# Kernel optimization log

Measured on AMD Instinct MI355X. Metric: run time of the kernel, lower is better.

Reference implementation:

```python
import jax, jax.numpy as jnp
import numpy as np
from jax import lax

DN = ('NCHW', 'OIHW', 'NCHW')

def _conv(x, w, b, stride):
    y = lax.conv_general_dilated(x, w, (stride, stride), [(1, 1), (1, 1)], dimension_numbers=DN)
    return y + b[None, :, None, None]

def _deconv(x, w, b):
    # ConvTranspose2d(k=4, stride=2, pad=1) == conv with lhs_dilation=2, pad=k-1-p=2,
    # with w already in flipped OIHW layout.
    y = lax.conv_general_dilated(x, w, (1, 1), [(2, 2), (2, 2)], lhs_dilation=(2, 2), dimension_numbers=DN)
    return y + b[None, :, None, None]

def setup_inputs() -> dict:
    key = jax.random.key(0)
    ks = jax.random.split(key, 14)
    s = 0.05  # keep activations numerically tame
    return {
        'x':   jax.random.normal(ks[0], (16, 3, 256, 256), jnp.float32),
        'ew1': jax.random.normal(ks[1], (64, 3, 4, 4), jnp.float32) * s,
        'eb1': jax.random.normal(ks[2], (64,), jnp.float32) * s,
        'ew2': jax.random.normal(ks[3], (128, 64, 4, 4), jnp.float32) * s,
        'eb2': jax.random.normal(ks[4], (128,), jnp.float32) * s,
        'ew3': jax.random.normal(ks[5], (256, 128, 4, 4), jnp.float32) * s,
        'eb3': jax.random.normal(ks[6], (256,), jnp.float32) * s,
        'cb':  jax.random.normal(ks[7], (8192, 256), jnp.float32),
        'dw1': jax.random.normal(ks[8], (128, 256, 4, 4), jnp.float32) * s,
        'db1': jax.random.normal(ks[9], (128,), jnp.float32) * s,
        'dw2': jax.random.normal(ks[10], (64, 128, 4, 4), jnp.float32) * s,
        'db2': jax.random.normal(ks[11], (64,), jnp.float32) * s,
        'dw3': jax.random.normal(ks[12], (3, 64, 4, 4), jnp.float32) * s,
        'db3': jax.random.normal(ks[13], (3,), jnp.float32) * s,
    }

def reference(x, ew1, eb1, ew2, eb2, ew3, eb3, cb, dw1, db1, dw2, db2, dw3, db3):
    # encoder: 3 stride-2 convs with ReLU between
    h = jax.nn.relu(_conv(x, ew1, eb1, 2))
    h = jax.nn.relu(_conv(h, ew2, eb2, 2))
    feat = _conv(h, ew3, eb3, 2)                     # [B, 256, 32, 32]
    B, C, H, W = feat.shape
    flat = feat.reshape(B, C, H * W).transpose(0, 2, 1)  # [B, HW, C]
    scores = jnp.einsum('btc,kc->btk', flat, cb)     # [B, HW, K] large matrix
    indices = jnp.argmax(scores, axis=-1)            # [B, HW]
    quantized = cb[indices]                          # [B, HW, C]
    q = quantized.transpose(0, 2, 1).reshape(B, C, H, W)
    # decoder: 3 stride-2 transposed convs with ReLU between
    d = jax.nn.relu(_deconv(q, dw1, db1))
    d = jax.nn.relu(_deconv(d, dw2, db2))
    recon = _deconv(d, dw3, db3)                     # [B, 3, 256, 256]
    return recon, indices
```

## Files before the change

kernel.cpp:

```cpp
#include <hip/hip_runtime.h>
#include <hip/hip_fp16.h>
#include <cstdint>
#include <cstddef>

typedef __attribute__((ext_vector_type(8))) short short8;
typedef __attribute__((ext_vector_type(8))) _Float16 h16x8;
typedef __attribute__((ext_vector_type(4))) float f32x4;

__device__ __forceinline__ short f2bf(float x) {
  union { float f; unsigned u; } a; a.f = x;
  unsigned r = a.u + 0x7fff + ((a.u >> 16) & 1);
  return (short)(r >> 16);
}
__device__ __forceinline__ float bf2f(short s) {
  union { unsigned u; float f; } a;
  a.u = ((unsigned)(unsigned short)s) << 16; return a.f;
}
__device__ __forceinline__ void fsplit16(float v, short& h, short& l) {
  __half a = __float2half(v);
  h = (short)__half_as_ushort(a);
  l = (short)__half_as_ushort(__float2half(v - __half2float(a)));
}

__device__ __forceinline__ void ld16(const void* g, void* l) {
  __builtin_amdgcn_global_load_lds(
      (const __attribute__((address_space(1))) unsigned int*)g,
      (__attribute__((address_space(3))) unsigned int*)l, 16, 0, 0);
}

__global__ __launch_bounds__(256) void conv1_kernel(
    const float* __restrict__ x, const float* __restrict__ w,
    const float* __restrict__ bias, short* __restrict__ yh, short* __restrict__ yl)
{
  __shared__ __align__(16) float wl[64 * 48];
  __shared__ float bl[64];
  const int tid = threadIdx.x;
  for (int i = tid; i < 64 * 48; i += 256) wl[i] = w[i];
  if (tid < 64) bl[tid] = bias[tid];
  __syncthreads();
  const int n  = blockIdx.y;
  const int oh = blockIdx.x * 2 + (tid >> 7);
  const int ow = tid & 127;
  const float* xb = x + (size_t)n * 3 * 65536;
  const int ih0 = oh * 2 - 1, iw0 = ow * 2 - 1;
  float xin[48];
#pragma unroll
  for (int ic = 0; ic < 3; ++ic)
#pragma unroll
    for (int kh = 0; kh < 4; ++kh) {
      int ih = ih0 + kh;
      bool rok = (unsigned)ih < 256u;
#pragma unroll
      for (int kw = 0; kw < 4; ++kw) {
        int iw = iw0 + kw;
        xin[ic * 16 + kh * 4 + kw] =
            (rok && (unsigned)iw < 256u) ? xb[ic * 65536 + ih * 256 + iw] : 0.f;
      }
    }
  const size_t ob = ((size_t)n * 16384 + oh * 128 + ow) * 64;
  for (int g = 0; g < 8; ++g) {
    short hs[8], ls[8];
#pragma unroll
    for (int j = 0; j < 8; ++j) {
      const int oc = g * 8 + j;
      float acc = bl[oc];
      const float* wo = &wl[oc * 48];
#pragma unroll
      for (int t = 0; t < 48; ++t) acc = fmaf(wo[t], xin[t], acc);
      acc = fmaxf(acc, 0.f) * 64.f;
      fsplit16(acc, hs[j], ls[j]);
    }
    *(short8*)(yh + ob + g * 8) = *(short8*)hs;
    *(short8*)(yl + ob + g * 8) = *(short8*)ls;
  }
}

template <int COUT, int CIN>
__global__ __launch_bounds__(256) void wpack_conv(
    const float* __restrict__ w, short* __restrict__ Wh, short* __restrict__ Wl)
{
  constexpr int K = 16 * CIN;
  const int idx = blockIdx.x * 256 + threadIdx.x;
  const int oc = idx / K, k = idx - oc * K;
  const int kk = k / CIN, ic = k - kk * CIN;
  const int kh = kk >> 2, kw = kk & 3;
  float v = w[(((size_t)oc * CIN + ic) * 4 + kh) * 4 + kw] * 64.f;
  short h, l;
  fsplit16(v, h, l);
  Wh[idx] = h;
  Wl[idx] = l;
}

template <int CIN, int HIN, int COUTT, bool RELU, bool OUTF>
__global__ __launch_bounds__(256) void conv_mfma(
    const short* __restrict__ inh, const short* __restrict__ inl,
    const short* __restrict__ Wph, const short* __restrict__ Wpl,
    const float* __restrict__ bias,
    short* __restrict__ outh, short* __restrict__ outl,
    float* __restrict__ outf)
{
  constexpr int K = 16 * CIN;
  constexpr int HOUT = HIN / 2;
  constexpr int MT = 128, NPX = 128;
  constexpr int GS = (HOUT == 64) ? 6 : 5;
  constexpr int AE = 4 * MT, BE = 4 * NPX;
  constexpr float RS = 1.f / 4096.f;
  __shared__ __align__(16) short AhL[AE * 8];
  __shared__ __align__(16) short AlL[AE * 8];
  __shared__ __align__(16) short BhL[BE * 8];
  __shared__ __align__(16) short BlL[BE * 8];
  __shared__ __align__(16) float bl[MT];
  const int tid = threadIdx.x;
  const int w = tid >> 6, lane = tid & 63;
  const int wm = w >> 1, wn = w & 1;
  const int kgl = lane >> 4, cl = lane & 15;
  const int n = blockIdx.z;
  const int oc0 = blockIdx.y * MT;
  const int oh0 = blockIdx.x * (NPX / HOUT);
  if (tid < MT) bl[tid] = bias[oc0 + tid];

  f32x4 acc[4][4];
#pragma unroll
  for (int i = 0; i < 4; ++i)
#pragma unroll
    for (int j = 0; j < 4; ++j) acc[i][j] = (f32x4){0.f, 0.f, 0.f, 0.f};

  for (int kc = 0; kc < K; kc += 32) {
    const int kk = kc / CIN, ic0 = kc % CIN;
    const int kh = kk >> 2, kw = kk & 3;
    __syncthreads();
#pragma unroll
    for (int rep = 0; rep < AE / 256; ++rep) {
      int e = rep * 256 + tid;
      int kg = e >> 7, oc_l = e & (MT - 1);
      size_t go = (size_t)(oc0 + oc_l) * K + kc + kg * 8;
      int lo = (e & ~63) * 8;
      ld16(Wph + go, AhL + lo);
      ld16(Wpl + go, AlL + lo);
    }
#pragma unroll
    for (int rep = 0; rep < BE / 256; ++rep) {
      int e = rep * 256 + tid;
      int kg = e >> 7, m = e & (NPX - 1);
      int ih = 2 * (oh0 + (m >> GS)) - 1 + kh;
      int iw = 2 * (m & (HOUT - 1)) - 1 + kw;
      bool ok = ((unsigned)ih < (unsigned)HIN) && ((unsigned)iw < (unsigned)HIN);
      size_t go = ok ? ((size_t)((n * HIN + ih) * HIN + iw) * CIN + ic0 + kg * 8)
                     : (size_t)(ic0 + kg * 8);
      int lo = (e & ~63) * 8;
      ld16(inh + go, BhL + lo);
      ld16(inl + go, BlL + lo);
    }
    __syncthreads();
    h16x8 ah[4], al[4], bh[4], blv[4];
#pragma unroll
    for (int mt = 0; mt < 4; ++mt) {
      int row = kgl * MT + wm * 64 + mt * 16 + cl;
      ah[mt] = *(const h16x8*)&AhL[row * 8];
      al[mt] = *(const h16x8*)&AlL[row * 8];
    }
    const h16x8 zz = {0, 0, 0, 0, 0, 0, 0, 0};
#pragma unroll
    for (int nt = 0; nt < 4; ++nt) {
      int m = wn * 64 + nt * 16 + cl;
      int row = kgl * NPX + m;
      h16x8 vh = *(const h16x8*)&BhL[row * 8];
      h16x8 vl = *(const h16x8*)&BlL[row * 8];
      int ih = 2 * (oh0 + (m >> GS)) - 1 + kh;
      int iw = 2 * (m & (HOUT - 1)) - 1 + kw;
      bool ok = ((unsigned)ih < (unsigned)HIN) && ((unsigned)iw < (unsigned)HIN);
      bh[nt] = ok ? vh : zz;
      blv[nt] = ok ? vl : zz;
    }
#pragma unroll
    for (int mt = 0; mt < 4; ++mt)
#pragma unroll
      for (int nt = 0; nt < 4; ++nt) {
        acc[mt][nt] = __builtin_amdgcn_mfma_f32_16x16x32_f16(
            ah[mt], bh[nt], acc[mt][nt], 0, 0, 0);
        acc[mt][nt] = __builtin_amdgcn_mfma_f32_16x16x32_f16(
            ah[mt], blv[nt], acc[mt][nt], 0, 0, 0);
        acc[mt][nt] = __builtin_amdgcn_mfma_f32_16x16x32_f16(
            al[mt], bh[nt], acc[mt][nt], 0, 0, 0);
      }
  }
#pragma unroll
  for (int mt = 0; mt < 4; ++mt) {
    const int oc = wm * 64 + mt * 16 + kgl * 4;
    const float4 bv = *(const float4*)&bl[oc];
#pragma unroll
    for (int nt = 0; nt < 4; ++nt) {
      const int px = wn * 64 + nt * 16 + cl;
      const int oh = oh0 + (px >> GS), ow = px & (HOUT - 1);
      const size_t ob =
          ((size_t)n * (HOUT * HOUT) + oh * HOUT + ow) * COUTT + oc0 + oc;
      float v0 = acc[mt][nt][0] * RS + bv.x;
      float v1 = acc[mt][nt][1] * RS + bv.y;
      float v2 = acc[mt][nt][2] * RS + bv.z;
      float v3 = acc[mt][nt][3] * RS + bv.w;
      if (RELU) {
        v0 = fmaxf(v0, 0.f); v1 = fmaxf(v1, 0.f);
        v2 = fmaxf(v2, 0.f); v3 = fmaxf(v3, 0.f);
      }
      if constexpr (OUTF) {
        ushort4 s;
        s.x = __half_as_ushort(__float2half(v0));
        s.y = __half_as_ushort(__float2half(v1));
        s.z = __half_as_ushort(__float2half(v2));
        s.w = __half_as_ushort(__float2half(v3));
        *(ushort4*)((unsigned short*)outh + ob) = s;
        *(float4*)(outf + ob) = make_float4(v0, v1, v2, v3);
      } else {
        short4 hh, ll;
        fsplit16(v0 * 64.f, hh.x, ll.x);
        fsplit16(v1 * 64.f, hh.y, ll.y);
        fsplit16(v2 * 64.f, hh.z, ll.z);
        fsplit16(v3 * 64.f, hh.w, ll.w);
        *(short4*)(outh + ob) = hh;
        *(short4*)(outl + ob) = ll;
      }
    }
  }
}

__global__ __launch_bounds__(256) void cb_convert(
    const float* __restrict__ cb, short* __restrict__ cbh,
    short* __restrict__ cbl, short* __restrict__ cb16)
{
  const int g = blockIdx.x * 256 + threadIdx.x;
  const float* p = cb + (size_t)g * 8;
  short hs[8], ls[8], fs[8];
#pragma unroll
  for (int u = 0; u < 8; ++u) {
    float v = p[u];
    short h = f2bf(v);
    hs[u] = h;
    ls[u] = f2bf(v - bf2f(h));
    fs[u] = (short)__half_as_ushort(__float2half(v));
  }
  *(short8*)(cbh + (size_t)g * 8) = *(short8*)hs;
  *(short8*)(cbl + (size_t)g * 8) = *(short8*)ls;
  *(short8*)(cb16 + (size_t)g * 8) = *(short8*)fs;
}

__global__ __launch_bounds__(256) void vq_mfma(
    const short* __restrict__ cb16, const short* __restrict__ ft16,
    float2* __restrict__ pval, int2* __restrict__ pidx)
{
  __shared__ __align__(16) short Ah[4 * 128 * 8];
  __shared__ __align__(16) short Bh[4 * 128 * 8];
  const int tid = threadIdx.x;
  const int w = tid >> 6, lane = tid & 63;
  const int wm = w >> 1, wn = w & 1;
  const int tg = blockIdx.x, cg = blockIdx.y;
  const int code0 = cg * 128, tok0 = tg * 128;
  const int kgl = lane >> 4, cl = lane & 15;

  f32x4 acc[4][4];
#pragma unroll
  for (int i = 0; i < 4; ++i)
#pragma unroll
    for (int j = 0; j < 4; ++j) acc[i][j] = (f32x4){0.f, 0.f, 0.f, 0.f};

  const int i0 = w * 128;
  for (int kc = 0; kc < 256; kc += 32) {
    __syncthreads();
#pragma unroll
    for (int rep = 0; rep < 2; ++rep) {
      int ib = i0 + rep * 64;
      int i = ib + lane;
      int m = i & 127, kg = i >> 7;
      size_t goffA = (size_t)(code0 + m) * 256 + kc + kg * 8;
      size_t goffB = (size_t)(tok0 + m) * 256 + kc + kg * 8;
      int loff = ib * 8;
      ld16(cb16 + goffA, Ah + loff);
      ld16(ft16 + goffB, Bh + loff);
    }
    __syncthreads();
    h16x8 ah[4], bh[4];
#pragma unroll
    for (int mt = 0; mt < 4; ++mt) {
      int row = wm * 64 + mt * 16 + cl;
      ah[mt] = *(const h16x8*)&Ah[(kgl * 128 + row) * 8];
    }
#pragma unroll
    for (int nt = 0; nt < 4; ++nt) {
      int row = wn * 64 + nt * 16 + cl;
      bh[nt] = *(const h16x8*)&Bh[(kgl * 128 + row) * 8];
    }
#pragma unroll
    for (int mt = 0; mt < 4; ++mt)
#pragma unroll
      for (int nt = 0; nt < 4; ++nt)
        acc[mt][nt] = __builtin_amdgcn_mfma_f32_16x16x32_f16(
            ah[mt], bh[nt], acc[mt][nt], 0, 0, 0);
  }
  __syncthreads();

  float* Sv = (float*)Ah;
  int* Si = (int*)Bh;
#pragma unroll
  for (int nt = 0; nt < 4; ++nt) {
    float v1 = -3.4e38f, v2 = -3.4e38f;
    int j1 = 0, j2 = 0;
#pragma unroll
    for (int mt = 0; mt < 4; ++mt) {
      int cb2 = code0 + wm * 64 + mt * 16 + kgl * 4;
      f32x4 a = acc[mt][nt];
#pragma unroll
      for (int r = 0; r < 4; ++r) {
        float val = a[r];
        int code = cb2 + r;
        if (val > v1) { v2 = v1; j2 = j1; v1 = val; j1 = code; }
        else if (val > v2) { v2 = val; j2 = code; }
      }
    }
    for (int mk = 16; mk < 64; mk <<= 1) {
      float ov1 = __shfl_xor(v1, mk);
      int oj1 = __shfl_xor(j1, mk);
      float ov2 = __shfl_xor(v2, mk);
      int oj2 = __shfl_xor(j2, mk);
      if (ov1 > v1) {
        if (v1 >= ov2) { v2 = v1; j2 = j1; } else { v2 = ov2; j2 = oj2; }
        v1 = ov1; j1 = oj1;
      } else if (ov1 > v2) { v2 = ov1; j2 = oj1; }
    }
    if (lane < 16) {
      int tl = wn * 64 + nt * 16 + lane;
      Sv[(wm * 128 + tl) * 2 + 0] = v1;
      Sv[(wm * 128 + tl) * 2 + 1] = v2;
      Si[(wm * 128 + tl) * 2 + 0] = j1;
      Si[(wm * 128 + tl) * 2 + 1] = j2;
    }
  }
  __syncthreads();
  if (tid < 128) {
    int tl = tid;
    float v1 = Sv[tl * 2], v2 = Sv[tl * 2 + 1];
    int j1 = Si[tl * 2], j2 = Si[tl * 2 + 1];
    float ov1 = Sv[(128 + tl) * 2], ov2 = Sv[(128 + tl) * 2 + 1];
    int oj1 = Si[(128 + tl) * 2], oj2 = Si[(128 + tl) * 2 + 1];
    if (ov1 > v1) {
      if (v1 >= ov2) { v2 = v1; j2 = j1; } else { v2 = ov2; j2 = oj2; }
      v1 = ov1; j1 = oj1;
    } else if (ov1 > v2) { v2 = ov1; j2 = oj1; }
    size_t o = (size_t)cg * 16384 + tok0 + tl;
    pval[o] = make_float2(v1, v2);
    pidx[o] = make_int2(j1, j2);
  }
}

__global__ __launch_bounds__(256) void vq_rescore(
    const float2* __restrict__ pval, const int2* __restrict__ pidx,
    const float* __restrict__ featc, const float* __restrict__ cb,
    int* __restrict__ fidx, float* __restrict__ idx_out)
{
  const int t = blockIdx.x * 256 + threadIdx.x;
  float vs[4] = {-3.4e38f, -3.4e38f, -3.4e38f, -3.4e38f};
  int is[4] = {0, 0, 0, 0};
  for (int cgi = 0; cgi < 64; ++cgi) {
    float2 pv = pval[(size_t)cgi * 16384 + t];
    int2 pi = pidx[(size_t)cgi * 16384 + t];
#pragma unroll
    for (int s = 0; s < 2; ++s) {
      float v = s ? pv.y : pv.x;
      int ii = s ? pi.y : pi.x;
      if (v > vs[3]) {
        vs[3] = v; is[3] = ii;
#pragma unroll
        for (int k = 3; k > 0; --k)
          if (vs[k] > vs[k - 1]) {
            float tv = vs[k]; vs[k] = vs[k - 1]; vs[k - 1] = tv;
            int ti = is[k]; is[k] = is[k - 1]; is[k - 1] = ti;
          }
      }
    }
  }
  const float4* fc = (const float4*)(featc + (size_t)t * 256);
  const float4* c0 = (const float4*)(cb + (size_t)is[0] * 256);
  const float4* c1 = (const float4*)(cb + (size_t)is[1] * 256);
  const float4* c2 = (const float4*)(cb + (size_t)is[2] * 256);
  const float4* c3 = (const float4*)(cb + (size_t)is[3] * 256);
  float s0 = 0.f, s1 = 0.f, s2 = 0.f, s3 = 0.f;
  for (int k4 = 0; k4 < 64; ++k4) {
    float4 f = fc[k4];
    float4 w0 = c0[k4], w1 = c1[k4], w2 = c2[k4], w3 = c3[k4];
    s0 = fmaf(w0.x, f.x, fmaf(w0.y, f.y, fmaf(w0.z, f.z, fmaf(w0.w, f.w, s0))));
    s1 = fmaf(w1.x, f.x, fmaf(w1.y, f.y, fmaf(w1.z, f.z, fmaf(w1.w, f.w, s1))));
    s2 = fmaf(w2.x, f.x, fmaf(w2.y, f.y, fmaf(w2.z, f.z, fmaf(w2.w, f.w, s2))));
    s3 = fmaf(w3.x, f.x, fmaf(w3.y, f.y, fmaf(w3.z, f.z, fmaf(w3.w, f.w, s3))));
  }
  float best = s0; int bi = is[0];
  float sv[3] = {s1, s2, s3};
  int si2[3] = {is[1], is[2], is[3]};
#pragma unroll
  for (int c = 0; c < 3; ++c)
    if (sv[c] > best || (sv[c] == best && si2[c] < bi)) { best = sv[c]; bi = si2[c]; }
  fidx[t] = bi;
  idx_out[t] = (float)bi;
}

template <int COUT, int CIN>
__global__ __launch_bounds__(256) void wpack(
    const float* __restrict__ w, short* __restrict__ Ah, short* __restrict__ Al)
{
  constexpr int K = 4 * CIN;
  const int idx = blockIdx.x * 256 + threadIdx.x;
  const int par = idx / (COUT * K);
  const int rem = idx % (COUT * K);
  const int oc = rem / K;
  const int k = rem % K;
  const int kk = k / CIN, ic = k % CIN;
  const int kh = 2 * (kk >> 1) + (par >> 1);
  const int kw = 2 * (kk & 1) + (par & 1);
  float v = w[(((size_t)oc * CIN + ic) * 4 + kh) * 4 + kw];
  short h = f2bf(v);
  Ah[idx] = h;
  Al[idx] = f2bf(v - bf2f(h));
}

__global__ __launch_bounds__(256) void zfill(float4* __restrict__ p) {
  p[threadIdx.x] = make_float4(0.f, 0.f, 0.f, 0.f);
}

__global__ __launch_bounds__(256) void gather2(
    const short* __restrict__ cbh, const short* __restrict__ cbl,
    const int* __restrict__ fidx, short* __restrict__ qTh, short* __restrict__ qTl)
{
  const int tid = threadIdx.x;
  const int gt = blockIdx.x * 64 + (tid >> 2);
  const int part = tid & 3;
  const int code = fidx[gt];
  const short8* sh = (const short8*)(cbh + (size_t)code * 256 + part * 64);
  const short8* sl = (const short8*)(cbl + (size_t)code * 256 + part * 64);
  short8* dh = (short8*)(qTh + (size_t)gt * 256 + part * 64);
  short8* dl = (short8*)(qTl + (size_t)gt * 256 + part * 64);
#pragma unroll
  for (int j = 0; j < 8; ++j) { dh[j] = sh[j]; dl[j] = sl[j]; }
}

template <int CIN, int GRID, int COUT, int NPX, int WM, int WN, bool OUT_HALF>
__global__ __launch_bounds__(256) void deconv_mfma(
    const short* __restrict__ inh, const short* __restrict__ inl,
    const short* __restrict__ Aph, const short* __restrict__ Apl,
    const float* __restrict__ bias, void* __restrict__ out_h,
    void* __restrict__ out_l, const short* __restrict__ zp)
{
  constexpr int K = 4 * CIN, HOUT = 2 * GRID, AE = 4 * COUT, BE = 4 * NPX;
  constexpr int GS = (GRID == 32) ? 5 : 6;
  __shared__ __align__(16) short AhL[AE * 8];
  __shared__ __align__(16) short AlL[AE * 8];
  __shared__ __align__(16) short BhL[BE * 8];
  __shared__ __align__(16) short BlL[BE * 8];
  __shared__ float bl[COUT];
  const int tid = threadIdx.x;
  const int w = tid >> 6, lane = tid & 63;
  const int wm = w / WN, wn = w % WN;
  const int kgl = lane >> 4, cl = lane & 15;
  const int par = blockIdx.y, n = blockIdx.z;
  const int pr = par >> 1, pc = par & 1;
  const int Ut0 = blockIdx.x * (NPX / GRID);
  if (tid < COUT) bl[tid] = bias[tid];

  f32x4 acc[4][4];
#pragma unroll
  for (int i = 0; i < 4; ++i)
#pragma unroll
    for (int j = 0; j < 4; ++j) acc[i][j] = (f32x4){0.f, 0.f, 0.f, 0.f};

  for (int kc = 0; kc < K; kc += 32) {
    const int kk = kc / CIN, ic0 = kc % CIN;
    const int dr = (kk >> 1) + pr - 1, dc = (kk & 1) + pc - 1;
    __syncthreads();
#pragma unroll
    for (int rep = 0; rep < AE / 256; ++rep) {
      int e = rep * 256 + tid;
      int kg = e / COUT, oc_l = e % COUT;
      size_t go = ((size_t)(par * COUT + oc_l)) * K + kc + kg * 8;
      int lo = (e & ~63) * 8;
      ld16(Aph + go, AhL + lo);
      ld16(Apl + go, AlL + lo);
    }
#pragma unroll
    for (int rep = 0; rep < BE / 256; ++rep) {
      int e = rep * 256 + tid;
      int kg = e / NPX, m = e % NPX;
      int sU = Ut0 + (m >> GS) + dr;
      int sV = (m & (GRID - 1)) + dc;
      bool ok = (unsigned)sU < (unsigned)GRID && (unsigned)sV < (unsigned)GRID;
      long pix = (long)(n * GRID + sU) * GRID + sV;
      size_t go = (size_t)(pix * CIN + ic0 + kg * 8);
      int lo = (e & ~63) * 8;
      ld16(ok ? inh + go : zp, BhL + lo);
      ld16(ok ? inl + go : zp, BlL + lo);
    }
    __syncthreads();
    short8 ah[4], al[4], bh[4], blo[4];
#pragma unroll
    for (int mt = 0; mt < 4; ++mt) {
      int row = kgl * COUT + wm * 64 + mt * 16 + cl;
      ah[mt] = *(const short8*)&AhL[row * 8];
      al[mt] = *(const short8*)&AlL[row * 8];
    }
#pragma unroll
    for (int nt = 0; nt < 4; ++nt) {
      int row = kgl * NPX + wn * 64 + nt * 16 + cl;
      bh[nt] = *(const short8*)&BhL[row * 8];
      blo[nt] = *(const short8*)&BlL[row * 8];
    }
#pragma unroll
    for (int mt = 0; mt < 4; ++mt)
#pragma unroll
      for (int nt = 0; nt < 4; ++nt) {
        acc[mt][nt] = __builtin_amdgcn_mfma_f32_16x16x32_bf16(
            ah[mt], bh[nt], acc[mt][nt], 0, 0, 0);
        acc[mt][nt] = __builtin_amdgcn_mfma_f32_16x16x32_bf16(
            ah[mt], blo[nt], acc[mt][nt], 0, 0, 0);
        acc[mt][nt] = __builtin_amdgcn_mfma_f32_16x16x32_bf16(
            al[mt], bh[nt], acc[mt][nt], 0, 0, 0);
      }
  }
#pragma unroll
  for (int mt = 0; mt < 4; ++mt) {
    const int oc = wm * 64 + mt * 16 + kgl * 4;
    const float4 bv = *(const float4*)&bl[oc];
#pragma unroll
    for (int nt = 0; nt < 4; ++nt) {
      const int px = wn * 64 + nt * 16 + cl;
      const int U = Ut0 + (px >> GS), V = px & (GRID - 1);
      const int r = 2 * U + pr, c = 2 * V + pc;
      const size_t ob = ((size_t)n * HOUT * HOUT + (size_t)r * HOUT + c) * COUT + oc;
      float v0 = fmaxf(acc[mt][nt][0] + bv.x, 0.f);
      float v1 = fmaxf(acc[mt][nt][1] + bv.y, 0.f);
      float v2 = fmaxf(acc[mt][nt][2] + bv.z, 0.f);
      float v3 = fmaxf(acc[mt][nt][3] + bv.w, 0.f);
      if constexpr (OUT_HALF) {
        ushort4 s;
        s.x = __half_as_ushort(__float2half(v0));
        s.y = __half_as_ushort(__float2half(v1));
        s.z = __half_as_ushort(__float2half(v2));
        s.w = __half_as_ushort(__float2half(v3));
        *(ushort4*)((unsigned short*)out_h + ob) = s;
      } else {
        short4 hh, ll;
        hh.x = f2bf(v0); ll.x = f2bf(v0 - bf2f(hh.x));
        hh.y = f2bf(v1); ll.y = f2bf(v1 - bf2f(hh.y));
        hh.z = f2bf(v2); ll.z = f2bf(v2 - bf2f(hh.z));
        hh.w = f2bf(v3); ll.w = f2bf(v3 - bf2f(hh.w));
        *(short4*)((short*)out_h + ob) = hh;
        *(short4*)((short*)out_l + ob) = ll;
      }
    }
  }
}

__global__ __launch_bounds__(256) void deconv3_kernel(
    const __half* __restrict__ d2, const float* __restrict__ w,
    const float* __restrict__ bias, float* __restrict__ y)
{
  __shared__ __align__(16) float Xl[108 * 68];
  __shared__ __align__(16) float wl[4 * 4 * 3 * 64];
  const int tid = threadIdx.x;
  for (int i = tid; i < 3072; i += 256) {
    int oc = i >> 10, ic = (i >> 4) & 63, kh = (i >> 2) & 3, kw = i & 3;
    int par = (kh & 1) * 2 + (kw & 1), kidx = (kh >> 1) * 2 + (kw >> 1);
    wl[((par * 4 + kidx) * 3 + oc) * 64 + ic] = w[i];
  }
  const int n = blockIdx.z, r0 = blockIdx.y * 8, c0 = blockIdx.x * 32;
  const int gr0 = (r0 >> 1) - 1, gc0 = (c0 >> 1) - 1;
  for (int e = tid; e < 1728; e += 256) {
    int pl = e >> 4, sub = e & 15;
    int rr = pl / 18, cc = pl - rr * 18;
    int gr = gr0 + rr, gc = gc0 + cc;
    float4 v = make_float4(0.f, 0.f, 0.f, 0.f);
    if ((unsigned)gr < 128u && (unsigned)gc < 128u) {
      const __half2* p =
          (const __half2*)(d2 + ((size_t)(n * 16384 + gr * 128 + gc) * 64 + sub * 4));
      float2 f0 = __half22float2(p[0]);
      float2 f1 = __half22float2(p[1]);
      v = make_float4(f0.x, f0.y, f1.x, f1.y);
    }
    *(float4*)&Xl[pl * 68 + sub * 4] = v;
  }
  __syncthreads();
  const int wv = tid >> 6, lane = tid & 63;
  const int pr = wv >> 1, pc = wv & 1;
  const int Ul = lane >> 4, Vl = lane & 15;
  float a0 = bias[0], a1 = bias[1], a2 = bias[2];
  const int parb = wv * 768;
#pragma unroll
  for (int ic4 = 0; ic4 < 16; ++ic4) {
    float4 xv[4];
#pragma unroll
    for (int t = 0; t < 4; ++t) {
      int lr = Ul + (t >> 1) + pr, lc = Vl + (t & 1) + pc;
      xv[t] = *(const float4*)&Xl[(lr * 18 + lc) * 68 + ic4 * 4];
    }
#pragma unroll
    for (int t = 0; t < 4; ++t) {
      float4 w0 = *(const float4*)&wl[parb + (t * 3 + 0) * 64 + ic4 * 4];
      float4 w1 = *(const float4*)&wl[parb + (t * 3 + 1) * 64 + ic4 * 4];
      float4 w2 = *(const float4*)&wl[parb + (t * 3 + 2) * 64 + ic4 * 4];
      a0 = fmaf(w0.x, xv[t].x, fmaf(w0.y, xv[t].y, fmaf(w0.z, xv[t].z, fmaf(w0.w, xv[t].w, a0))));
      a1 = fmaf(w1.x, xv[t].x, fmaf(w1.y, xv[t].y, fmaf(w1.z, xv[t].z, fmaf(w1.w, xv[t].w, a1))));
      a2 = fmaf(w2.x, xv[t].x, fmaf(w2.y, xv[t].y, fmaf(w2.z, xv[t].z, fmaf(w2.w, xv[t].w, a2))));
    }
  }
  const int r = r0 + 2 * Ul + pr, c = c0 + 2 * Vl + pc;
  float* yn = y + (size_t)n * 3 * 65536 + r * 256 + c;
  yn[0] = a0;
  yn[65536] = a1;
  yn[131072] = a2;
}

extern "C" void kernel_launch(void* const* d_in, const int* in_sizes, int n_in,
                              void* d_out, int out_size, void* d_ws, size_t ws_size,
                              hipStream_t stream)
{
  const float* x   = (const float*)d_in[0];
  const float* ew1 = (const float*)d_in[1];
  const float* eb1 = (const float*)d_in[2];
  const float* ew2 = (const float*)d_in[3];
  const float* eb2 = (const float*)d_in[4];
  const float* ew3 = (const float*)d_in[5];
  const float* eb3 = (const float*)d_in[6];
  const float* cb  = (const float*)d_in[7];
  const float* dw1 = (const float*)d_in[8];
  const float* db1 = (const float*)d_in[9];
  const float* dw2 = (const float*)d_in[10];
  const float* db2 = (const float*)d_in[11];
  const float* dw3 = (const float*)d_in[12];
  const float* db3 = (const float*)d_in[13];

  float* recon = (float*)d_out;
  float* idxf  = (float*)d_out + 3145728;

  const size_t MB = 1048576ull;
  char* ws = (char*)d_ws;
  short* h1h = (short*)ws;
  short* h1l = (short*)(ws + 32 * MB);
  short* h2h = (short*)(ws + 64 * MB);
  short* h2l = (short*)(ws + 80 * MB);
  short* ft16  = (short*)ws;
  float* featf = (float*)(ws + 16 * MB);
  short* cbh  = (short*)(ws + 64 * MB);
  short* cbl  = (short*)(ws + 68 * MB);
  short* cb16 = (short*)(ws + 72 * MB);
  float2* pval = (float2*)(ws + 76 * MB);
  int2*   pidx = (int2*)(ws + 84 * MB);
  int*    fidx = (int*)(ws + 92 * MB);
  short* A1h = (short*)(ws + 76 * MB);
  short* A1l = (short*)(ws + 77 * MB);
  short* A2h = (short*)(ws + 78 * MB);
  short* A2l = (short*)(ws + 78 * MB + 262144);
  short* zp  = (short*)(ws + 78 * MB + 524288);
  short* qTh = (short*)ws;
  short* qTl = (short*)(ws + 8 * MB);
  short* d1h = (short*)(ws + 32 * MB);
  short* d1l = (short*)(ws + 48 * MB);
  __half* d2 = (__half*)ws;
  short* W2h = (short*)recon;
  short* W2l = W2h + 131072;
  short* W3h = W2h + 262144;
  short* W3l = W2h + 786432;

  conv1_kernel<<<dim3(64, 16), 256, 0, stream>>>(x, ew1, eb1, h1h, h1l);
  wpack_conv<128, 64><<<dim3(512), 256, 0, stream>>>(ew2, W2h, W2l);
  conv_mfma<64, 128, 128, true, false><<<dim3(32, 1, 16), 256, 0, stream>>>(
      h1h, h1l, W2h, W2l, eb2, h2h, h2l, nullptr);
  wpack_conv<256, 128><<<dim3(2048), 256, 0, stream>>>(ew3, W3h, W3l);
  conv_mfma<128, 64, 256, false, true><<<dim3(8, 2, 16), 256, 0, stream>>>(
      h2h, h2l, W3h, W3l, eb3, ft16, nullptr, featf);

  cb_convert<<<dim3(1024), 256, 0, stream>>>(cb, cbh, cbl, cb16);
  vq_mfma<<<dim3(128, 64), 256, 0, stream>>>(cb16, ft16, pval, pidx);
  vq_rescore<<<dim3(64), 256, 0, stream>>>(pval, pidx, featf, cb, fidx, idxf);

  wpack<128, 256><<<dim3(2048), 256, 0, stream>>>(dw1, A1h, A1l);
  wpack<64, 128><<<dim3(512), 256, 0, stream>>>(dw2, A2h, A2l);
  zfill<<<dim3(1), 256, 0, stream>>>((float4*)zp);
  gather2<<<dim3(256), 256, 0, stream>>>(cbh, cbl, fidx, qTh, qTl);

  deconv_mfma<256, 32, 128, 128, 2, 2, false>
      <<<dim3(8, 4, 16), 256, 0, stream>>>(qTh, qTl, A1h, A1l, db1, d1h, d1l, zp);
  deconv_mfma<128, 64, 64, 256, 1, 4, true>
      <<<dim3(16, 4, 16), 256, 0, stream>>>(d1h, d1l, A2h, A2l, db2, d2, d2, zp);
  deconv3_kernel<<<dim3(8, 32, 16), 256, 0, stream>>>(d2, dw3, db3, recon);
}
```

Measured before the change: 900.9 us.

## Double-buffer weight tiles and load activations directly into registers in MFMA convs

The conv, deconv and VQ MFMA kernels now keep two shared-memory buffers for the weight/codebook tiles, so the next K-slice is loaded while the current one is computed, with one barrier per stage instead of two. In the conv and deconv kernels the activation (B) operand no longer goes through shared memory; each lane reads its fragments straight from global memory into registers and zeroes out-of-bounds taps. This also removes the zero-page buffer and its zfill launch. The cost is more registers and more shared memory per block, and uncoalesced, repeated global reads of activations that may lower occupancy or raise memory traffic.

```diff
diff --git a/kernel.cpp b/kernel.cpp
--- a/kernel.cpp
+++ b/kernel.cpp
@@ -103,12 +103,11 @@
   constexpr int HOUT = HIN / 2;
   constexpr int MT = 128, NPX = 128;
   constexpr int GS = (HOUT == 64) ? 6 : 5;
-  constexpr int AE = 4 * MT, BE = 4 * NPX;
+  constexpr int AE = 4 * MT;
+  constexpr int NS = K / 32;
   constexpr float RS = 1.f / 4096.f;
-  __shared__ __align__(16) short AhL[AE * 8];
-  __shared__ __align__(16) short AlL[AE * 8];
-  __shared__ __align__(16) short BhL[BE * 8];
-  __shared__ __align__(16) short BlL[BE * 8];
+  __shared__ __align__(16) short AhL[2][AE * 8];
+  __shared__ __align__(16) short AlL[2][AE * 8];
   __shared__ __align__(16) float bl[MT];
   const int tid = threadIdx.x;
   const int w = tid >> 6, lane = tid & 63;
@@ -125,52 +124,44 @@
 #pragma unroll
     for (int j = 0; j < 4; ++j) acc[i][j] = (f32x4){0.f, 0.f, 0.f, 0.f};
 
-  for (int kc = 0; kc < K; kc += 32) {
-    const int kk = kc / CIN, ic0 = kc % CIN;
-    const int kh = kk >> 2, kw = kk & 3;
-    __syncthreads();
+  auto stageA = [&](int s, int b) {
+    const int kc = s * 32;
 #pragma unroll
     for (int rep = 0; rep < AE / 256; ++rep) {
       int e = rep * 256 + tid;
       int kg = e >> 7, oc_l = e & (MT - 1);
       size_t go = (size_t)(oc0 + oc_l) * K + kc + kg * 8;
       int lo = (e & ~63) * 8;
-      ld16(Wph + go, AhL + lo);
-      ld16(Wpl + go, AlL + lo);
-    }
-#pragma unroll
-    for (int rep = 0; rep < BE / 256; ++rep) {
-      int e = rep * 256 + tid;
-      int kg = e >> 7, m = e & (NPX - 1);
+      ld16(Wph + go, &AhL[b][lo]);
+      ld16(Wpl + go, &AlL[b][lo]);
+    }
+  };
+  const h16x8 zzh = {0, 0, 0, 0, 0, 0, 0, 0};
+  auto loadB = [&](int s, h16x8* bh, h16x8* blv) {
+    const int kc = s * 32;
+    const int kk = kc / CIN, ic0 = kc % CIN;
+    const int kh = kk >> 2, kw = kk & 3;
+#pragma unroll
+    for (int nt = 0; nt < 4; ++nt) {
+      int m = wn * 64 + nt * 16 + cl;
       int ih = 2 * (oh0 + (m >> GS)) - 1 + kh;
       int iw = 2 * (m & (HOUT - 1)) - 1 + kw;
       bool ok = ((unsigned)ih < (unsigned)HIN) && ((unsigned)iw < (unsigned)HIN);
-      size_t go = ok ? ((size_t)((n * HIN + ih) * HIN + iw) * CIN + ic0 + kg * 8)
-                     : (size_t)(ic0 + kg * 8);
-      int lo = (e & ~63) * 8;
-      ld16(inh + go, BhL + lo);
-      ld16(inl + go, BlL + lo);
-    }
-    __syncthreads();
-    h16x8 ah[4], al[4], bh[4], blv[4];
+      size_t go = ok ? ((size_t)((n * HIN + ih) * HIN + iw) * CIN + ic0 + kgl * 8)
+                     : (size_t)(ic0 + kgl * 8);
+      h16x8 vh = *(const h16x8*)(inh + go);
+      h16x8 vl = *(const h16x8*)(inl + go);
+      bh[nt] = ok ? vh : zzh;
+      blv[nt] = ok ? vl : zzh;
+    }
+  };
+  auto compute = [&](int b, const h16x8* bh, const h16x8* blv) {
+    h16x8 ah[4], al[4];
 #pragma unroll
     for (int mt = 0; mt < 4; ++mt) {
       int row = kgl * MT + wm * 64 + mt * 16 + cl;
-      ah[mt] = *(const h16x8*)&AhL[row * 8];
-      al[mt] = *(const h16x8*)&AlL[row * 8];
-    }
-    const h16x8 zz = {0, 0, 0, 0, 0, 0, 0, 0};
-#pragma unroll
-    for (int nt = 0; nt < 4; ++nt) {
-      int m = wn * 64 + nt * 16 + cl;
-      int row = kgl * NPX + m;
-      h16x8 vh = *(const h16x8*)&BhL[row * 8];
-      h16x8 vl = *(const h16x8*)&BlL[row * 8];
-      int ih = 2 * (oh0 + (m >> GS)) - 1 + kh;
-      int iw = 2 * (m & (HOUT - 1)) - 1 + kw;
-      bool ok = ((unsigned)ih < (unsigned)HIN) && ((unsigned)iw < (unsigned)HIN);
-      bh[nt] = ok ? vh : zz;
-      blv[nt] = ok ? vl : zz;
+      ah[mt] = *(const h16x8*)&AhL[b][row * 8];
+      al[mt] = *(const h16x8*)&AlL[b][row * 8];
     }
 #pragma unroll
     for (int mt = 0; mt < 4; ++mt)
@@ -183,6 +174,20 @@
         acc[mt][nt] = __builtin_amdgcn_mfma_f32_16x16x32_f16(
             al[mt], bh[nt], acc[mt][nt], 0, 0, 0);
       }
+  };
+
+  h16x8 bhA[4], blA[4], bhB[4], blB[4];
+  stageA(0, 0);
+  loadB(0, bhA, blA);
+  __syncthreads();
+  for (int s2 = 0; s2 < NS; s2 += 2) {
+    stageA(s2 + 1, 1);
+    loadB(s2 + 1, bhB, blB);
+    compute(0, bhA, blA);
+    __syncthreads();
+    if (s2 + 2 < NS) { stageA(s2 + 2, 0); loadB(s2 + 2, bhA, blA); }
+    compute(1, bhB, blB);
+    __syncthreads();
   }
 #pragma unroll
   for (int mt = 0; mt < 4; ++mt) {
@@ -247,8 +252,8 @@
     const short* __restrict__ cb16, const short* __restrict__ ft16,
     float2* __restrict__ pval, int2* __restrict__ pidx)
 {
-  __shared__ __align__(16) short Ah[4 * 128 * 8];
-  __shared__ __align__(16) short Bh[4 * 128 * 8];
+  __shared__ __align__(16) short Ah[2][4 * 128 * 8];
+  __shared__ __align__(16) short Bh[2][4 * 128 * 8];
   const int tid = threadIdx.x;
   const int w = tid >> 6, lane = tid & 63;
   const int wm = w >> 1, wn = w & 1;
@@ -263,8 +268,8 @@
     for (int j = 0; j < 4; ++j) acc[i][j] = (f32x4){0.f, 0.f, 0.f, 0.f};
 
   const int i0 = w * 128;
-  for (int kc = 0; kc < 256; kc += 32) {
-    __syncthreads();
+  auto stage = [&](int s, int b) {
+    const int kc = s * 32;
 #pragma unroll
     for (int rep = 0; rep < 2; ++rep) {
       int ib = i0 + rep * 64;
@@ -273,20 +278,21 @@
       size_t goffA = (size_t)(code0 + m) * 256 + kc + kg * 8;
       size_t goffB = (size_t)(tok0 + m) * 256 + kc + kg * 8;
       int loff = ib * 8;
-      ld16(cb16 + goffA, Ah + loff);
-      ld16(ft16 + goffB, Bh + loff);
-    }
-    __syncthreads();
+      ld16(cb16 + goffA, &Ah[b][loff]);
+      ld16(ft16 + goffB, &Bh[b][loff]);
+    }
+  };
+  auto compute = [&](int b) {
     h16x8 ah[4], bh[4];
 #pragma unroll
     for (int mt = 0; mt < 4; ++mt) {
       int row = wm * 64 + mt * 16 + cl;
-      ah[mt] = *(const h16x8*)&Ah[(kgl * 128 + row) * 8];
+      ah[mt] = *(const h16x8*)&Ah[b][(kgl * 128 + row) * 8];
     }
 #pragma unroll
     for (int nt = 0; nt < 4; ++nt) {
       int row = wn * 64 + nt * 16 + cl;
-      bh[nt] = *(const h16x8*)&Bh[(kgl * 128 + row) * 8];
+      bh[nt] = *(const h16x8*)&Bh[b][(kgl * 128 + row) * 8];
     }
 #pragma unroll
     for (int mt = 0; mt < 4; ++mt)
@@ -294,11 +300,21 @@
       for (int nt = 0; nt < 4; ++nt)
         acc[mt][nt] = __builtin_amdgcn_mfma_f32_16x16x32_f16(
             ah[mt], bh[nt], acc[mt][nt], 0, 0, 0);
-  }
+  };
+
+  stage(0, 0);
   __syncthreads();
-
-  float* Sv = (float*)Ah;
-  int* Si = (int*)Bh;
+  for (int s2 = 0; s2 < 8; s2 += 2) {
+    stage(s2 + 1, 1);
+    compute(0);
+    __syncthreads();
+    if (s2 + 2 < 8) stage(s2 + 2, 0);
+    compute(1);
+    __syncthreads();
+  }
+
+  float* Sv = (float*)&Ah[0][0];
+  int* Si = (int*)&Bh[0][0];
 #pragma unroll
   for (int nt = 0; nt < 4; ++nt) {
     float v1 = -3.4e38f, v2 = -3.4e38f;
@@ -419,10 +435,6 @@
   Al[idx] = f2bf(v - bf2f(h));
 }
 
-__global__ __launch_bounds__(256) void zfill(float4* __restrict__ p) {
-  p[threadIdx.x] = make_float4(0.f, 0.f, 0.f, 0.f);
-}
-
 __global__ __launch_bounds__(256) void gather2(
     const short* __restrict__ cbh, const short* __restrict__ cbl,
     const int* __restrict__ fidx, short* __restrict__ qTh, short* __restrict__ qTl)
@@ -444,14 +456,13 @@
     const short* __restrict__ inh, const short* __restrict__ inl,
     const short* __restrict__ Aph, const short* __restrict__ Apl,
     const float* __restrict__ bias, void* __restrict__ out_h,
-    void* __restrict__ out_l, const short* __restrict__ zp)
-{
-  constexpr int K = 4 * CIN, HOUT = 2 * GRID, AE = 4 * COUT, BE = 4 * NPX;
+    void* __restrict__ out_l)
+{
+  constexpr int K = 4 * CIN, HOUT = 2 * GRID, AE = 4 * COUT;
   constexpr int GS = (GRID == 32) ? 5 : 6;
-  __shared__ __align__(16) short AhL[AE * 8];
-  __shared__ __align__(16) short AlL[AE * 8];
-  __shared__ __align__(16) short BhL[BE * 8];
-  __shared__ __align__(16) short BlL[BE * 8];
+  constexpr int NS = K / 32;
+  __shared__ __align__(16) short AhL[2][AE * 8];
+  __shared__ __align__(16) short AlL[2][AE * 8];
   __shared__ float bl[COUT];
   const int tid = threadIdx.x;
   const int w = tid >> 6, lane = tid & 63;
@@ -468,45 +479,45 @@
 #pragma unroll
     for (int j = 0; j < 4; ++j) acc[i][j] = (f32x4){0.f, 0.f, 0.f, 0.f};
 
-  for (int kc = 0; kc < K; kc += 32) {
-    const int kk = kc / CIN, ic0 = kc % CIN;
-    const int dr = (kk >> 1) + pr - 1, dc = (kk & 1) + pc - 1;
-    __syncthreads();
+  auto stageA = [&](int s, int b) {
+    const int kc = s * 32;
 #pragma unroll
     for (int rep = 0; rep < AE / 256; ++rep) {
       int e = rep * 256 + tid;
       int kg = e / COUT, oc_l = e % COUT;
       size_t go = ((size_t)(par * COUT + oc_l)) * K + kc + kg * 8;
       int lo = (e & ~63) * 8;
-      ld16(Aph + go, AhL + lo);
-      ld16(Apl + go, AlL + lo);
-    }
-#pragma unroll
-    for (int rep = 0; rep < BE / 256; ++rep) {
-      int e = rep * 256 + tid;
-      int kg = e / NPX, m = e % NPX;
+      ld16(Aph + go, &AhL[b][lo]);
+      ld16(Apl + go, &AlL[b][lo]);
+    }
+  };
+  const short8 zz = {0, 0, 0, 0, 0, 0, 0, 0};
+  auto loadB = [&](int s, short8* bh, short8* blo) {
+    const int kc = s * 32;
+    const int kk = kc / CIN, ic0 = kc % CIN;
+    const int dr = (kk >> 1) + pr - 1, dc = (kk & 1) + pc - 1;
+#pragma unroll
+    for (int nt = 0; nt < 4; ++nt) {
+      int m = wn * 64 + nt * 16 + cl;
       int sU = Ut0 + (m >> GS) + dr;
       int sV = (m & (GRID - 1)) + dc;
       bool ok = (unsigned)sU < (unsigned)GRID && (unsigned)sV < (unsigned)GRID;
       long pix = (long)(n * GRID + sU) * GRID + sV;
-      size_t go = (size_t)(pix * CIN + ic0 + kg * 8);
-      int lo = (e & ~63) * 8;
-      ld16(ok ? inh + go : zp, BhL + lo);
-      ld16(ok ? inl + go : zp, BlL + lo);
-    }
-    __syncthreads();
-    short8 ah[4], al[4], bh[4], blo[4];
+      size_t go = ok ? (size_t)(pix * CIN + ic0 + kgl * 8)
+                     : (size_t)(ic0 + kgl * 8);
+      short8 vh = *(const short8*)(inh + go);
+      short8 vl = *(const short8*)(inl + go);
+      bh[nt] = ok ? vh : zz;
+      blo[nt] = ok ? vl : zz;
+    }
+  };
+  auto compute = [&](int b, const short8* bh, const short8* blo) {
+    short8 ah[4], al[4];
 #pragma unroll
     for (int mt = 0; mt < 4; ++mt) {
       int row = kgl * COUT + wm * 64 + mt * 16 + cl;
-      ah[mt] = *(const short8*)&AhL[row * 8];
-      al[mt] = *(const short8*)&AlL[row * 8];
-    }
-#pragma unroll
-    for (int nt = 0; nt < 4; ++nt) {
-      int row = kgl * NPX + wn * 64 + nt * 16 + cl;
-      bh[nt] = *(const short8*)&BhL[row * 8];
-      blo[nt] = *(const short8*)&BlL[row * 8];
+      ah[mt] = *(const short8*)&AhL[b][row * 8];
+      al[mt] = *(const short8*)&AlL[b][row * 8];
     }
 #pragma unroll
     for (int mt = 0; mt < 4; ++mt)
@@ -519,6 +530,20 @@
         acc[mt][nt] = __builtin_amdgcn_mfma_f32_16x16x32_bf16(
             al[mt], bh[nt], acc[mt][nt], 0, 0, 0);
       }
+  };
+
+  short8 bhA[4], blA[4], bhB[4], blB[4];
+  stageA(0, 0);
+  loadB(0, bhA, blA);
+  __syncthreads();
+  for (int s2 = 0; s2 < NS; s2 += 2) {
+    stageA(s2 + 1, 1);
+    loadB(s2 + 1, bhB, blB);
+    compute(0, bhA, blA);
+    __syncthreads();
+    if (s2 + 2 < NS) { stageA(s2 + 2, 0); loadB(s2 + 2, bhA, blA); }
+    compute(1, bhB, blB);
+    __syncthreads();
   }
 #pragma unroll
   for (int mt = 0; mt < 4; ++mt) {
@@ -653,7 +678,6 @@
   short* A1l = (short*)(ws + 77 * MB);
   short* A2h = (short*)(ws + 78 * MB);
   short* A2l = (short*)(ws + 78 * MB + 262144);
-  short* zp  = (short*)(ws + 78 * MB + 524288);
   short* qTh = (short*)ws;
   short* qTl = (short*)(ws + 8 * MB);
   short* d1h = (short*)(ws + 32 * MB);
@@ -678,12 +702,11 @@
 
   wpack<128, 256><<<dim3(2048), 256, 0, stream>>>(dw1, A1h, A1l);
   wpack<64, 128><<<dim3(512), 256, 0, stream>>>(dw2, A2h, A2l);
-  zfill<<<dim3(1), 256, 0, stream>>>((float4*)zp);
   gather2<<<dim3(256), 256, 0, stream>>>(cbh, cbl, fidx, qTh, qTl);
 
   deconv_mfma<256, 32, 128, 128, 2, 2, false>
-      <<<dim3(8, 4, 16), 256, 0, stream>>>(qTh, qTl, A1h, A1l, db1, d1h, d1l, zp);
+      <<<dim3(8, 4, 16), 256, 0, stream>>>(qTh, qTl, A1h, A1l, db1, d1h, d1l);
   deconv_mfma<128, 64, 64, 256, 1, 4, true>
-      <<<dim3(16, 4, 16), 256, 0, stream>>>(d1h, d1l, A2h, A2l, db2, d2, d2, zp);
+      <<<dim3(16, 4, 16), 256, 0, stream>>>(d1h, d1l, A2h, A2l, db2, d2, d2);
   deconv3_kernel<<<dim3(8, 32, 16), 256, 0, stream>>>(d2, dw3, db3, recon);
 }
```

New measurement: 917.0 us. About the same (+1.8%).
